# Optimization experiments

Measured on AMD Instinct MI355X. Metric: run time of the kernel, lower is better.

## Reference

```python
import jax, jax.numpy as jnp
import numpy as np

W_GLOBAL, W_SOFT, W_HARD = 0.2, 0.3, 0.5
GAMMA, ALPHA = 2.0, 0.25
MIN_TEMP, MAX_TEMP = 0.01, 100.0
EPS = 1e-12


def _l2norm(x, axis):
    n = jnp.sqrt(jnp.sum(x * x, axis=axis, keepdims=True))
    return x / jnp.maximum(n, EPS)


def _focal_ce(logits, labels):
    # torch F.cross_entropy with label_smoothing=ALPHA, then focal modulation
    log_p = jax.nn.log_softmax(logits, axis=-1)           # (B, K)
    nll = -jnp.take_along_axis(log_p, labels[:, None], axis=-1)[:, 0]
    smooth = -jnp.mean(log_p, axis=-1)
    ce = (1.0 - ALPHA) * nll + ALPHA * smooth
    pt = jnp.exp(-ce)
    return jnp.mean((1.0 - pt) ** GAMMA * ce)


def setup_inputs() -> dict:
    key = jax.random.key(0)
    k1, k2, k3 = jax.random.split(key, 3)
    B, C, N = 256, 512, 512
    yolo_feats = jax.random.normal(k1, (B, C, N), dtype=jnp.float32)
    clip_feats = jax.random.normal(k2, (B, C), dtype=jnp.float32)
    logit_scale = jax.random.uniform(k3, (1,), dtype=jnp.float32) * 2.0 + 2.0
    return {"yolo_feats": yolo_feats, "clip_feats": clip_feats, "logit_scale": logit_scale}


def reference(yolo_feats, clip_feats, logit_scale):
    yolo_feats = _l2norm(yolo_feats, axis=1)              # (B, C, N)
    clip_feats = _l2norm(clip_feats, axis=1)              # (B, C)
    scale = jnp.clip(jnp.exp(logit_scale), MIN_TEMP, MAX_TEMP)  # (1,)
    B = yolo_feats.shape[0]
    labels = jnp.arange(B, dtype=jnp.int32)

    # global branch
    yolo_global = _l2norm(jnp.mean(yolo_feats, axis=2), axis=1)   # (B, C)
    sim_global = (yolo_global @ clip_feats.T) * scale             # (B, B)
    loss_global = 0.5 * (_focal_ce(sim_global, labels) + _focal_ce(sim_global.T, labels))

    # dense spatial similarity map (B, N, K=B)
    sim_map = jnp.einsum('bcn,kc->bnk', yolo_feats, clip_feats) * scale

    sim_soft = jax.nn.logsumexp(sim_map, axis=1)                  # (B, B)
    loss_soft = 0.5 * (_focal_ce(sim_soft, labels) + _focal_ce(sim_soft.T, labels))

    sim_hard = jnp.max(sim_map, axis=1)                           # (B, B)
    loss_hard = 0.5 * (_focal_ce(sim_hard, labels) + _focal_ce(sim_hard.T, labels))

    return W_GLOBAL * loss_global + W_SOFT * loss_soft + W_HARD * loss_hard
```

## Files before the change

kernel.cpp:

```cpp
#include <hip/hip_runtime.h>
#include <math.h>

constexpr int B = 256;
constexpr int C = 512;
constexpr int N = 512;
constexpr int K = 256;

constexpr size_t OFF_CLIPNB = 0;
constexpr size_t OFF_INV    = OFF_CLIPNB + (size_t)B*C/2;
constexpr size_t OFF_SGLOB  = OFF_INV   + (size_t)B*N;
constexpr size_t OFF_SSOFT  = OFF_SGLOB + (size_t)B*K;
constexpr size_t OFF_SHARD  = OFF_SSOFT + (size_t)B*K;
constexpr size_t OFF_PM     = OFF_SHARD + (size_t)B*K;
constexpr size_t OFF_PS     = OFF_PM    + (size_t)2*B*K;
constexpr size_t OFF_PH     = OFF_PS    + (size_t)2*B*K;
constexpr size_t OFF_PG     = OFF_PH    + (size_t)2*B*K;
constexpr size_t OFF_GN     = OFF_PG    + (size_t)2*B*K;
constexpr size_t OFF_MISC   = OFF_GN    + (size_t)B;

typedef __attribute__((ext_vector_type(8))) short short8;
typedef __attribute__((ext_vector_type(4))) float f32x4;

__device__ __forceinline__ float wave_reduce_sum(float v) {
  #pragma unroll
  for (int off = 32; off > 0; off >>= 1) v += __shfl_xor(v, off, 64);
  return v;
}
__device__ __forceinline__ float wave_reduce_max(float v) {
  #pragma unroll
  for (int off = 32; off > 0; off >>= 1) v = fmaxf(v, __shfl_xor(v, off, 64));
  return v;
}
__device__ __forceinline__ unsigned int bf16_rne(float x) {
  unsigned int u = __builtin_bit_cast(unsigned int, x);
  return (u + 0x7FFFu + ((u >> 16) & 1u)) >> 16;
}
__device__ __forceinline__ unsigned int pk_bf16(float x, float y) {
  return bf16_rne(x) | (bf16_rne(y) << 16);
}

__global__ void k_misc(const float* __restrict__ ls, float* __restrict__ misc) {
  int t = threadIdx.x;
  if (t == 0) misc[0] = fminf(fmaxf(expf(ls[0]), 0.01f), 100.0f);
  if (t >= 1 && t < 7) misc[t] = 0.0f;
}

__global__ __launch_bounds__(256) void k_rownorm(const float* __restrict__ src,
                                                 unsigned short* __restrict__ dst_bf) {
  int b = blockIdx.x, t = threadIdx.x;
  float x0 = src[(size_t)b * C + t];
  float x1 = src[(size_t)b * C + t + 256];
  __shared__ float red[4];
  float w = wave_reduce_sum(x0 * x0 + x1 * x1);
  if ((t & 63) == 0) red[t >> 6] = w;
  __syncthreads();
  float tot = red[0] + red[1] + red[2] + red[3];
  float r = 1.0f / fmaxf(sqrtf(tot), 1e-12f);
  dst_bf[(size_t)b * C + t] = (unsigned short)bf16_rne(x0 * r);
  dst_bf[(size_t)b * C + t + 256] = (unsigned short)bf16_rne(x1 * r);
}

__global__ __launch_bounds__(256, 2) void k_main_mfma(
    const float* __restrict__ yolo,
    const unsigned short* __restrict__ clipnb,
    const float* __restrict__ misc,
    float* __restrict__ invg,
    float* __restrict__ PM, float* __restrict__ PS, float* __restrict__ PH,
    float* __restrict__ PG) {
  int bh = blockIdx.x;
  int b = bh >> 1, half = bh & 1;
  int t = threadIdx.x;
  int w = t >> 6, lane = t & 63;
  int quad = lane >> 4, col = lane & 15;

  __shared__ unsigned int xl[128 * 32];
  __shared__ float ssqb[8 * 128];
  __shared__ float invt[128];

  const float scale = misc[0];
  const float* ybase = yolo + (size_t)b * C * N;

  int nf = t & 31;
  int cp0 = t >> 5;
  unsigned int rotv = (8u * (nf & 3) + 4u * (unsigned)(nf >> 2)) & 31u;

  float msk[16], ssk[16], hsk[16];
  #pragma unroll
  for (int i = 0; i < 16; i++) { msk[i] = -1e30f; ssk[i] = 0.f; hsk[i] = -1e30f; }

  for (int iter = 0; iter < 2; iter++) {
    int n0 = half * 256 + iter * 128;
    float4 ssq4 = {0.f, 0.f, 0.f, 0.f};

    f32x4 acc[4][8];
    #pragma unroll
    for (int kt = 0; kt < 4; kt++)
      #pragma unroll
      for (int nt = 0; nt < 8; nt++) {
        f32x4 z = {0.f, 0.f, 0.f, 0.f};
        acc[kt][nt] = z;
      }

    for (int cc = 0; cc < 8; cc++) {
      int c0 = cc * 64;
      __syncthreads();

      short8 afr[4][2];
      #pragma unroll
      for (int kt = 0; kt < 4; kt++)
        #pragma unroll
        for (int s = 0; s < 2; s++) {
          const unsigned short* ap =
              clipnb + (size_t)(64 * w + 16 * kt + col) * C + c0 + 32 * s + 8 * quad;
          union { uint4 u; short8 v; } fa;
          fa.u = *(const uint4*)ap;
          afr[kt][s] = fa.v;
        }

      #pragma unroll
      for (int p = 0; p < 4; p++) {
        int cp = cp0 + 8 * p;
        int c = c0 + 2 * cp;
        const float* pa = ybase + (size_t)c * N + n0 + 4 * nf;
        float4 a = *(const float4*)pa;
        float4 bb = *(const float4*)(pa + N);
        ssq4.x += a.x * a.x + bb.x * bb.x;
        ssq4.y += a.y * a.y + bb.y * bb.y;
        ssq4.z += a.z * a.z + bb.z * bb.z;
        ssq4.w += a.w * a.w + bb.w * bb.w;
        unsigned int pos = ((unsigned)cp + rotv) & 31u;
        int base0 = (4 * nf) * 32;
        xl[base0 + pos]       = pk_bf16(a.x, bb.x);
        xl[base0 + 32 + pos]  = pk_bf16(a.y, bb.y);
        xl[base0 + 64 + pos]  = pk_bf16(a.z, bb.z);
        xl[base0 + 96 + pos]  = pk_bf16(a.w, bb.w);
      }
      __syncthreads();

      #pragma unroll
      for (int s = 0; s < 2; s++) {
        #pragma unroll
        for (int nt = 0; nt < 8; nt++) {
          int n = 16 * nt + col;
          unsigned int pos =
              (unsigned)(16 * s + 4 * quad + 8 * (col >> 2) + 4 * nt) & 31u;
          union { uint4 u; short8 v; } fb;
          fb.u = *(const uint4*)&xl[n * 32 + pos];
          #pragma unroll
          for (int kt = 0; kt < 4; kt++)
            acc[kt][nt] = __builtin_amdgcn_mfma_f32_16x16x32_bf16(
                afr[kt][s], fb.v, acc[kt][nt], 0, 0, 0);
        }
      }
    }

    {
      int base = cp0 * 128 + 4 * nf;
      ssqb[base + 0] = ssq4.x;
      ssqb[base + 1] = ssq4.y;
      ssqb[base + 2] = ssq4.z;
      ssqb[base + 3] = ssq4.w;
    }
    __syncthreads();
    if (t < 128) {
      float s = 0.f;
      #pragma unroll
      for (int g = 0; g < 8; g++) s += ssqb[g * 128 + t];
      float iv = 1.0f / fmaxf(sqrtf(s), 1e-12f);
      invt[t] = iv;
      invg[(size_t)b * N + n0 + t] = iv;
    }
    __syncthreads();

    float invn[8];
    #pragma unroll
    for (int nt = 0; nt < 8; nt++) invn[nt] = invt[16 * nt + col];
    #pragma unroll
    for (int kt = 0; kt < 4; kt++)
      #pragma unroll
      for (int r = 0; r < 4; r++) {
        int idx = kt * 4 + r;
        float mm = msk[idx], ss = ssk[idx], hh = hsk[idx], gg = 0.f;
        #pragma unroll
        for (int nt = 0; nt < 8; nt++) {
          float vu = acc[kt][nt][r] * invn[nt];
          gg += vu;
          float v = vu * scale;
          hh = fmaxf(hh, v);
          float M = fmaxf(mm, v);
          ss = ss * __expf(mm - M) + __expf(v - M);
          mm = M;
        }
        msk[idx] = mm; ssk[idx] = ss; hsk[idx] = hh;
        #pragma unroll
        for (int o = 1; o < 16; o <<= 1) gg += __shfl_xor(gg, o, 64);
        if (col == 0) {
          size_t a = (size_t)bh * 256 + (64 * w + 16 * kt + 4 * quad + r);
          if (iter == 0) PG[a] = gg; else PG[a] += gg;
        }
      }
  }

  #pragma unroll
  for (int idx = 0; idx < 16; idx++) {
    float mm = msk[idx], ss = ssk[idx], hh = hsk[idx];
    #pragma unroll
    for (int o = 1; o < 16; o <<= 1) {
      float mo = __shfl_xor(mm, o, 64);
      float so = __shfl_xor(ss, o, 64);
      float ho = __shfl_xor(hh, o, 64);
      float M = fmaxf(mm, mo);
      ss = ss * __expf(mm - M) + so * __expf(mo - M);
      mm = M;
      hh = fmaxf(hh, ho);
    }
    msk[idx] = mm; ssk[idx] = ss; hsk[idx] = hh;
  }
  if (col == 0) {
    size_t pbase = (size_t)bh * 256;
    #pragma unroll
    for (int kt = 0; kt < 4; kt++)
      #pragma unroll
      for (int r = 0; r < 4; r++) {
        int k = 64 * w + 16 * kt + 4 * quad + r;
        int idx = kt * 4 + r;
        PM[pbase + k] = msk[idx];
        PS[pbase + k] = ssk[idx];
        PH[pbase + k] = hsk[idx];
      }
  }
}

__global__ __launch_bounds__(512) void k_gnorm(const float* __restrict__ yolo,
                                               const float* __restrict__ invg,
                                               float* __restrict__ gn) {
  int b = blockIdx.x;
  int t = threadIdx.x;
  int w = t >> 6, lane = t & 63;
  const float* xb = yolo + (size_t)b * C * N;
  const float* ivb = invg + (size_t)b * N;
  float4 iv[2];
  #pragma unroll
  for (int p = 0; p < 2; p++) iv[p] = *(const float4*)(ivb + p * 256 + 4 * lane);
  float sq = 0.f;
  for (int ci = 0; ci < 64; ci++) {
    int c = w * 64 + ci;
    const float* row = xb + (size_t)c * N + 4 * lane;
    float cs = 0.f;
    #pragma unroll
    for (int p = 0; p < 2; p++) {
      float4 v = *(const float4*)(row + p * 256);
      cs += v.x * iv[p].x + v.y * iv[p].y + v.z * iv[p].z + v.w * iv[p].w;
    }
    cs = wave_reduce_sum(cs);
    sq += cs * cs;
  }
  __shared__ float red[8];
  if (lane == 0) red[w] = sq;
  __syncthreads();
  if (t == 0) {
    float s = 0.f;
    #pragma unroll
    for (int g = 0; g < 8; g++) s += red[g];
    gn[b] = fmaxf(sqrtf(s) * (1.0f / (float)N), 1e-12f);
  }
}

__global__ __launch_bounds__(256) void k_sglob(const float* __restrict__ PG,
                                               const float* __restrict__ gn,
                                               const float* __restrict__ misc,
                                               float* __restrict__ Sglob) {
  int i = blockIdx.x, k = threadIdx.x;
  float v = PG[(size_t)(2 * i) * 256 + k] + PG[(size_t)(2 * i + 1) * 256 + k];
  Sglob[(size_t)i * K + k] = misc[0] * v * (1.0f / (float)N) / gn[i];
}

__global__ __launch_bounds__(256) void k_merge(const float* __restrict__ PM,
                                               const float* __restrict__ PS,
                                               const float* __restrict__ PH,
                                               float* __restrict__ Ssoft,
                                               float* __restrict__ Shard) {
  int b = blockIdx.x, k = threadIdx.x;
  size_t p0 = (size_t)(2 * b) * 256 + k;
  size_t p1 = (size_t)(2 * b + 1) * 256 + k;
  float m0 = PM[p0], m1 = PM[p1];
  float M = fmaxf(m0, m1);
  float S = PS[p0] * __expf(m0 - M) + PS[p1] * __expf(m1 - M);
  Ssoft[(size_t)b * K + k] = M + __logf(S);
  Shard[(size_t)b * K + k] = fmaxf(PH[p0], PH[p1]);
}

__global__ __launch_bounds__(256) void k_focal(const float* __restrict__ Sglob,
                                               const float* __restrict__ Ssoft,
                                               const float* __restrict__ Shard,
                                               float* __restrict__ misc) {
  int job = blockIdx.y;
  int i = blockIdx.x;
  int t = threadIdx.x;
  const float* M = job < 2 ? Sglob : (job < 4 ? Ssoft : Shard);
  float v = (job & 1) ? M[(size_t)t * K + i] : M[(size_t)i * K + t];
  __shared__ float red[4];
  float mx = wave_reduce_max(v);
  if ((t & 63) == 0) red[t >> 6] = mx;
  __syncthreads();
  mx = fmaxf(fmaxf(red[0], red[1]), fmaxf(red[2], red[3]));
  __syncthreads();
  float sv = wave_reduce_sum(v);
  if ((t & 63) == 0) red[t >> 6] = sv;
  __syncthreads();
  float sumv = red[0] + red[1] + red[2] + red[3];
  __syncthreads();
  float se = wave_reduce_sum(expf(v - mx));
  if ((t & 63) == 0) red[t >> 6] = se;
  __syncthreads();
  if (t == 0) {
    float sumexp = red[0] + red[1] + red[2] + red[3];
    float logZ = mx + logf(sumexp);
    float diag = M[(size_t)i * K + i];
    float nll = logZ - diag;
    float smooth = logZ - sumv * (1.0f / 256.0f);
    float ce = 0.75f * nll + 0.25f * smooth;
    float pt = expf(-ce);
    float fo = (1.0f - pt) * (1.0f - pt) * ce;
    atomicAdd(&misc[1 + job], fo);
  }
}

__global__ void k_finish(const float* __restrict__ misc, float* __restrict__ out) {
  float lg = misc[1] + misc[2];
  float ls = misc[3] + misc[4];
  float lh = misc[5] + misc[6];
  out[0] = (0.2f * lg + 0.3f * ls + 0.5f * lh) * 0.5f * (1.0f / 256.0f);
}

extern "C" void kernel_launch(void* const* d_in, const int* in_sizes, int n_in,
                              void* d_out, int out_size, void* d_ws, size_t ws_size,
                              hipStream_t stream) {
  const float* yolo = (const float*)d_in[0];
  const float* clip = (const float*)d_in[1];
  const float* ls   = (const float*)d_in[2];
  float* out = (float*)d_out;
  float* ws = (float*)d_ws;
  unsigned short* clipnb = (unsigned short*)(ws + OFF_CLIPNB);
  float* invg  = ws + OFF_INV;
  float* Sglob = ws + OFF_SGLOB;
  float* Ssoft = ws + OFF_SSOFT;
  float* Shard = ws + OFF_SHARD;
  float* PM    = ws + OFF_PM;
  float* PS    = ws + OFF_PS;
  float* PH    = ws + OFF_PH;
  float* PG    = ws + OFF_PG;
  float* gn    = ws + OFF_GN;
  float* misc  = ws + OFF_MISC;

  k_misc<<<1, 64, 0, stream>>>(ls, misc);
  k_rownorm<<<256, 256, 0, stream>>>(clip, clipnb);
  k_main_mfma<<<512, 256, 0, stream>>>(yolo, clipnb, misc, invg, PM, PS, PH, PG);
  k_gnorm<<<256, 512, 0, stream>>>(yolo, invg, gn);
  k_sglob<<<256, 256, 0, stream>>>(PG, gn, misc, Sglob);
  k_merge<<<256, 256, 0, stream>>>(PM, PS, PH, Ssoft, Shard);
  k_focal<<<dim3(256, 6), 256, 0, stream>>>(Sglob, Ssoft, Shard, misc);
  k_finish<<<1, 1, 0, stream>>>(misc, out);
}
```

Before: 477.4 us.

## Stage full-C yolo windows in LDS, use 32x32 MFMA, fuse global-norm pass

The main kernel now splits each batch into four 128-column windows. Each block loads the whole C dimension of its window into LDS once as bf16 and computes the per-column inverse norms before the MFMA loop. The loop switches from 16x16x32 to 32x32x16 bf16 MFMA tiles, with no per-chunk syncs. The per-channel mean needed for the global branch is computed from the already staged LDS data, so the separate k_gnorm pass that re-read all of yolo from HBM is gone. The hard max is reused from the running max, so PH is no longer written. In exchange, merge kernels read 8 partials instead of 2, LDS use is much larger (128 KB), and the global mean now uses bf16-rounded values.

```diff
diff --git a/kernel.cpp b/kernel.cpp
--- a/kernel.cpp
+++ b/kernel.cpp
@@ -5,21 +5,21 @@
 constexpr int C = 512;
 constexpr int N = 512;
 constexpr int K = 256;
+constexpr int WIN = 128;
 
 constexpr size_t OFF_CLIPNB = 0;
-constexpr size_t OFF_INV    = OFF_CLIPNB + (size_t)B*C/2;
-constexpr size_t OFF_SGLOB  = OFF_INV   + (size_t)B*N;
+constexpr size_t OFF_SGLOB  = OFF_CLIPNB + (size_t)B*C/2;
 constexpr size_t OFF_SSOFT  = OFF_SGLOB + (size_t)B*K;
 constexpr size_t OFF_SHARD  = OFF_SSOFT + (size_t)B*K;
 constexpr size_t OFF_PM     = OFF_SHARD + (size_t)B*K;
-constexpr size_t OFF_PS     = OFF_PM    + (size_t)2*B*K;
-constexpr size_t OFF_PH     = OFF_PS    + (size_t)2*B*K;
-constexpr size_t OFF_PG     = OFF_PH    + (size_t)2*B*K;
-constexpr size_t OFF_GN     = OFF_PG    + (size_t)2*B*K;
+constexpr size_t OFF_PS     = OFF_PM    + (size_t)8*B*K;
+constexpr size_t OFF_PG     = OFF_PS    + (size_t)8*B*K;
+constexpr size_t OFF_S1     = OFF_PG    + (size_t)8*B*K;
+constexpr size_t OFF_GN     = OFF_S1    + (size_t)2048*512;
 constexpr size_t OFF_MISC   = OFF_GN    + (size_t)B;
 
-typedef __attribute__((ext_vector_type(8))) short short8;
-typedef __attribute__((ext_vector_type(4))) float f32x4;
+typedef __attribute__((ext_vector_type(8)))  short short8;
+typedef __attribute__((ext_vector_type(16))) float f32x16;
 
 __device__ __forceinline__ float wave_reduce_sum(float v) {
   #pragma unroll
@@ -60,208 +60,160 @@
   dst_bf[(size_t)b * C + t + 256] = (unsigned short)bf16_rne(x1 * r);
 }
 
-__global__ __launch_bounds__(256, 2) void k_main_mfma(
+__global__ __launch_bounds__(512, 2) void k_main2(
     const float* __restrict__ yolo,
     const unsigned short* __restrict__ clipnb,
     const float* __restrict__ misc,
-    float* __restrict__ invg,
-    float* __restrict__ PM, float* __restrict__ PS, float* __restrict__ PH,
-    float* __restrict__ PG) {
-  int bh = blockIdx.x;
-  int b = bh >> 1, half = bh & 1;
+    float* __restrict__ PM, float* __restrict__ PS, float* __restrict__ PG,
+    float* __restrict__ S1p) {
+  int bw = blockIdx.x;
+  int b = bw >> 2, win = bw & 3;
   int t = threadIdx.x;
   int w = t >> 6, lane = t & 63;
-  int quad = lane >> 4, col = lane & 15;
-
-  __shared__ unsigned int xl[128 * 32];
-  __shared__ float ssqb[8 * 128];
-  __shared__ float invt[128];
+  int half = lane >> 5, nl = lane & 31;
+  int kq = w & 3, ng = w >> 2;
+
+  __shared__ unsigned int xl[WIN * 256];
+  __shared__ float ssqb[16 * WIN];
+  __shared__ float invt[WIN];
 
   const float scale = misc[0];
-  const float* ybase = yolo + (size_t)b * C * N;
-
-  int nf = t & 31;
-  int cp0 = t >> 5;
-  unsigned int rotv = (8u * (nf & 3) + 4u * (unsigned)(nf >> 2)) & 31u;
-
-  float msk[16], ssk[16], hsk[16];
-  #pragma unroll
-  for (int i = 0; i < 16; i++) { msk[i] = -1e30f; ssk[i] = 0.f; hsk[i] = -1e30f; }
-
-  for (int iter = 0; iter < 2; iter++) {
-    int n0 = half * 256 + iter * 128;
+  const float* ybase = yolo + (size_t)b * C * N + win * WIN;
+
+  {
+    int nf = t & 31, cq = t >> 5;
+    int row = 4 * nf;
+    unsigned rw = 16u * (nf & 1) + 8u * ((nf >> 1) & 1);
     float4 ssq4 = {0.f, 0.f, 0.f, 0.f};
-
-    f32x4 acc[4][8];
+    #pragma unroll 4
+    for (int p = 0; p < 16; p++) {
+      int cp = cq + 16 * p;
+      const float* pa = ybase + (size_t)(2 * cp) * N + 4 * nf;
+      float4 a  = *(const float4*)pa;
+      float4 bb = *(const float4*)(pa + N);
+      ssq4.x += a.x * a.x + bb.x * bb.x;
+      ssq4.y += a.y * a.y + bb.y * bb.y;
+      ssq4.z += a.z * a.z + bb.z * bb.z;
+      ssq4.w += a.w * a.w + bb.w * bb.w;
+      int bhi = cp & ~31;
+      xl[(row + 0) * 256 + bhi + (int)(((unsigned)cp + rw +  0u) & 31u)] = pk_bf16(a.x, bb.x);
+      xl[(row + 1) * 256 + bhi + (int)(((unsigned)cp + rw +  4u) & 31u)] = pk_bf16(a.y, bb.y);
+      xl[(row + 2) * 256 + bhi + (int)(((unsigned)cp + rw +  8u) & 31u)] = pk_bf16(a.z, bb.z);
+      xl[(row + 3) * 256 + bhi + (int)(((unsigned)cp + rw + 12u) & 31u)] = pk_bf16(a.w, bb.w);
+    }
+    ssqb[cq * WIN + row + 0] = ssq4.x;
+    ssqb[cq * WIN + row + 1] = ssq4.y;
+    ssqb[cq * WIN + row + 2] = ssq4.z;
+    ssqb[cq * WIN + row + 3] = ssq4.w;
+  }
+  __syncthreads();
+  if (t < WIN) {
+    float s = 0.f;
     #pragma unroll
-    for (int kt = 0; kt < 4; kt++)
+    for (int g = 0; g < 16; g++) s += ssqb[g * WIN + t];
+    invt[t] = 1.0f / fmaxf(sqrtf(s), 1e-12f);
+  }
+  __syncthreads();
+
+  int kt0 = kq, kt1 = kq + 4;
+  int nt0 = 2 * ng, nt1 = 2 * ng + 1;
+  const unsigned short* a0p = clipnb + (size_t)(32 * kt0 + nl) * C + 8 * half;
+  const unsigned short* a1p = clipnb + (size_t)(32 * kt1 + nl) * C + 8 * half;
+  int brow0 = (32 * nt0 + nl) * 256;
+  int brow1 = (32 * nt1 + nl) * 256;
+  unsigned rotr = 4u * ((unsigned)(nl & 3) + 4u * ((nl >> 2) & 1) + 2u * ((nl >> 3) & 1));
+
+  f32x16 acc00, acc01, acc10, acc11;
+  #pragma unroll
+  for (int r = 0; r < 16; r++) { acc00[r] = 0.f; acc01[r] = 0.f; acc10[r] = 0.f; acc11[r] = 0.f; }
+
+  #pragma unroll 4
+  for (int step = 0; step < 32; step++) {
+    union { uint4 u; short8 v; } A0, A1, B0, B1;
+    A0.u = *(const uint4*)(a0p + 16 * step);
+    A1.u = *(const uint4*)(a1p + 16 * step);
+    int pos = 32 * (step >> 2) +
+              (int)(((unsigned)(8 * (step & 3) + 4 * half) + rotr) & 31u);
+    B0.u = *(const uint4*)&xl[brow0 + pos];
+    B1.u = *(const uint4*)&xl[brow1 + pos];
+    acc00 = __builtin_amdgcn_mfma_f32_32x32x16_bf16(A0.v, B0.v, acc00, 0, 0, 0);
+    acc01 = __builtin_amdgcn_mfma_f32_32x32x16_bf16(A0.v, B1.v, acc01, 0, 0, 0);
+    acc10 = __builtin_amdgcn_mfma_f32_32x32x16_bf16(A1.v, B0.v, acc10, 0, 0, 0);
+    acc11 = __builtin_amdgcn_mfma_f32_32x32x16_bf16(A1.v, B1.v, acc11, 0, 0, 0);
+  }
+
+  float ivr0 = invt[32 * nt0 + nl];
+  float ivr1 = invt[32 * nt1 + nl];
+  size_t pb = ((size_t)b * 8 + win * 2 + ng) * 256;
+  #pragma unroll
+  for (int tk = 0; tk < 2; tk++) {
+    int kbase = 32 * (tk ? kt1 : kt0);
+    #pragma unroll
+    for (int reg = 0; reg < 16; reg++) {
+      float u0 = (tk ? acc10[reg] : acc00[reg]) * ivr0;
+      float u1 = (tk ? acc11[reg] : acc01[reg]) * ivr1;
+      float v0 = u0 * scale, v1 = u1 * scale;
+      float M = fmaxf(v0, v1);
+      float G = u0 + u1;
       #pragma unroll
-      for (int nt = 0; nt < 8; nt++) {
-        f32x4 z = {0.f, 0.f, 0.f, 0.f};
-        acc[kt][nt] = z;
+      for (int o = 1; o < 32; o <<= 1) M = fmaxf(M, __shfl_xor(M, o, 64));
+      float e = __expf(v0 - M) + __expf(v1 - M);
+      #pragma unroll
+      for (int o = 1; o < 32; o <<= 1) {
+        e += __shfl_xor(e, o, 64);
+        G += __shfl_xor(G, o, 64);
       }
-
-    for (int cc = 0; cc < 8; cc++) {
-      int c0 = cc * 64;
-      __syncthreads();
-
-      short8 afr[4][2];
-      #pragma unroll
-      for (int kt = 0; kt < 4; kt++)
-        #pragma unroll
-        for (int s = 0; s < 2; s++) {
-          const unsigned short* ap =
-              clipnb + (size_t)(64 * w + 16 * kt + col) * C + c0 + 32 * s + 8 * quad;
-          union { uint4 u; short8 v; } fa;
-          fa.u = *(const uint4*)ap;
-          afr[kt][s] = fa.v;
-        }
-
-      #pragma unroll
-      for (int p = 0; p < 4; p++) {
-        int cp = cp0 + 8 * p;
-        int c = c0 + 2 * cp;
-        const float* pa = ybase + (size_t)c * N + n0 + 4 * nf;
-        float4 a = *(const float4*)pa;
-        float4 bb = *(const float4*)(pa + N);
-        ssq4.x += a.x * a.x + bb.x * bb.x;
-        ssq4.y += a.y * a.y + bb.y * bb.y;
-        ssq4.z += a.z * a.z + bb.z * bb.z;
-        ssq4.w += a.w * a.w + bb.w * bb.w;
-        unsigned int pos = ((unsigned)cp + rotv) & 31u;
-        int base0 = (4 * nf) * 32;
-        xl[base0 + pos]       = pk_bf16(a.x, bb.x);
-        xl[base0 + 32 + pos]  = pk_bf16(a.y, bb.y);
-        xl[base0 + 64 + pos]  = pk_bf16(a.z, bb.z);
-        xl[base0 + 96 + pos]  = pk_bf16(a.w, bb.w);
-      }
-      __syncthreads();
-
-      #pragma unroll
-      for (int s = 0; s < 2; s++) {
-        #pragma unroll
-        for (int nt = 0; nt < 8; nt++) {
-          int n = 16 * nt + col;
-          unsigned int pos =
-              (unsigned)(16 * s + 4 * quad + 8 * (col >> 2) + 4 * nt) & 31u;
-          union { uint4 u; short8 v; } fb;
-          fb.u = *(const uint4*)&xl[n * 32 + pos];
-          #pragma unroll
-          for (int kt = 0; kt < 4; kt++)
-            acc[kt][nt] = __builtin_amdgcn_mfma_f32_16x16x32_bf16(
-                afr[kt][s], fb.v, acc[kt][nt], 0, 0, 0);
-        }
+      if (nl == 0) {
+        int k = kbase + (reg & 3) + 8 * (reg >> 2) + 4 * half;
+        PM[pb + k] = M;
+        PS[pb + k] = e;
+        PG[pb + k] = G;
       }
     }
-
-    {
-      int base = cp0 * 128 + 4 * nf;
-      ssqb[base + 0] = ssq4.x;
-      ssqb[base + 1] = ssq4.y;
-      ssqb[base + 2] = ssq4.z;
-      ssqb[base + 3] = ssq4.w;
+  }
+
+  {
+    int cp2 = t >> 1, sub = t & 1;
+    int qhi = cp2 & ~31, qlo = cp2 & 31;
+    float s0 = 0.f, s1 = 0.f;
+    #pragma unroll 16
+    for (int i = 0; i < 64; i++) {
+      int n = 64 * sub + i;
+      unsigned rt = 4u * (unsigned)(i & 3) + 16u * ((i >> 2) & 1) + 8u * ((i >> 3) & 1);
+      unsigned dw = xl[n * 256 + qhi + (int)(((unsigned)qlo + rt) & 31u)];
+      float iv = invt[n];
+      float xlo = __builtin_bit_cast(float, dw << 16);
+      float xhi = __builtin_bit_cast(float, dw & 0xffff0000u);
+      s0 = fmaf(xlo, iv, s0);
+      s1 = fmaf(xhi, iv, s1);
     }
-    __syncthreads();
-    if (t < 128) {
-      float s = 0.f;
-      #pragma unroll
-      for (int g = 0; g < 8; g++) s += ssqb[g * 128 + t];
-      float iv = 1.0f / fmaxf(sqrtf(s), 1e-12f);
-      invt[t] = iv;
-      invg[(size_t)b * N + n0 + t] = iv;
-    }
-    __syncthreads();
-
-    float invn[8];
-    #pragma unroll
-    for (int nt = 0; nt < 8; nt++) invn[nt] = invt[16 * nt + col];
-    #pragma unroll
-    for (int kt = 0; kt < 4; kt++)
-      #pragma unroll
-      for (int r = 0; r < 4; r++) {
-        int idx = kt * 4 + r;
-        float mm = msk[idx], ss = ssk[idx], hh = hsk[idx], gg = 0.f;
-        #pragma unroll
-        for (int nt = 0; nt < 8; nt++) {
-          float vu = acc[kt][nt][r] * invn[nt];
-          gg += vu;
-          float v = vu * scale;
-          hh = fmaxf(hh, v);
-          float M = fmaxf(mm, v);
-          ss = ss * __expf(mm - M) + __expf(v - M);
-          mm = M;
-        }
-        msk[idx] = mm; ssk[idx] = ss; hsk[idx] = hh;
-        #pragma unroll
-        for (int o = 1; o < 16; o <<= 1) gg += __shfl_xor(gg, o, 64);
-        if (col == 0) {
-          size_t a = (size_t)bh * 256 + (64 * w + 16 * kt + 4 * quad + r);
-          if (iter == 0) PG[a] = gg; else PG[a] += gg;
-        }
-      }
-  }
-
-  #pragma unroll
-  for (int idx = 0; idx < 16; idx++) {
-    float mm = msk[idx], ss = ssk[idx], hh = hsk[idx];
-    #pragma unroll
-    for (int o = 1; o < 16; o <<= 1) {
-      float mo = __shfl_xor(mm, o, 64);
-      float so = __shfl_xor(ss, o, 64);
-      float ho = __shfl_xor(hh, o, 64);
-      float M = fmaxf(mm, mo);
-      ss = ss * __expf(mm - M) + so * __expf(mo - M);
-      mm = M;
-      hh = fmaxf(hh, ho);
-    }
-    msk[idx] = mm; ssk[idx] = ss; hsk[idx] = hh;
-  }
-  if (col == 0) {
-    size_t pbase = (size_t)bh * 256;
-    #pragma unroll
-    for (int kt = 0; kt < 4; kt++)
-      #pragma unroll
-      for (int r = 0; r < 4; r++) {
-        int k = 64 * w + 16 * kt + 4 * quad + r;
-        int idx = kt * 4 + r;
-        PM[pbase + k] = msk[idx];
-        PS[pbase + k] = ssk[idx];
-        PH[pbase + k] = hsk[idx];
-      }
-  }
-}
-
-__global__ __launch_bounds__(512) void k_gnorm(const float* __restrict__ yolo,
-                                               const float* __restrict__ invg,
-                                               float* __restrict__ gn) {
-  int b = blockIdx.x;
-  int t = threadIdx.x;
-  int w = t >> 6, lane = t & 63;
-  const float* xb = yolo + (size_t)b * C * N;
-  const float* ivb = invg + (size_t)b * N;
-  float4 iv[2];
-  #pragma unroll
-  for (int p = 0; p < 2; p++) iv[p] = *(const float4*)(ivb + p * 256 + 4 * lane);
-  float sq = 0.f;
-  for (int ci = 0; ci < 64; ci++) {
-    int c = w * 64 + ci;
-    const float* row = xb + (size_t)c * N + 4 * lane;
-    float cs = 0.f;
-    #pragma unroll
-    for (int p = 0; p < 2; p++) {
-      float4 v = *(const float4*)(row + p * 256);
-      cs += v.x * iv[p].x + v.y * iv[p].y + v.z * iv[p].z + v.w * iv[p].w;
-    }
-    cs = wave_reduce_sum(cs);
-    sq += cs * cs;
-  }
-  __shared__ float red[8];
-  if (lane == 0) red[w] = sq;
-  __syncthreads();
-  if (t == 0) {
+    size_t o = ((size_t)bw * 2 + sub) * 512 + 2 * cp2;
+    S1p[o] = s0;
+    S1p[o + 1] = s1;
+  }
+}
+
+__global__ __launch_bounds__(256) void k_gn2(const float* __restrict__ S1p,
+                                             float* __restrict__ gn) {
+  int b = blockIdx.x, t = threadIdx.x;
+  float tot = 0.f;
+  #pragma unroll
+  for (int cc = 0; cc < 2; cc++) {
+    int c = t + 256 * cc;
     float s = 0.f;
     #pragma unroll
-    for (int g = 0; g < 8; g++) s += red[g];
+    for (int wn = 0; wn < 4; wn++)
+      #pragma unroll
+      for (int sub = 0; sub < 2; sub++)
+        s += S1p[(((size_t)(b * 4 + wn)) * 2 + sub) * 512 + c];
+    tot += s * s;
+  }
+  __shared__ float red[4];
+  float wsum = wave_reduce_sum(tot);
+  if ((t & 63) == 0) red[t >> 6] = wsum;
+  __syncthreads();
+  if (t == 0) {
+    float s = red[0] + red[1] + red[2] + red[3];
     gn[b] = fmaxf(sqrtf(s) * (1.0f / (float)N), 1e-12f);
   }
 }
@@ -271,23 +223,28 @@
                                                const float* __restrict__ misc,
                                                float* __restrict__ Sglob) {
   int i = blockIdx.x, k = threadIdx.x;
-  float v = PG[(size_t)(2 * i) * 256 + k] + PG[(size_t)(2 * i + 1) * 256 + k];
+  float v = 0.f;
+  #pragma unroll
+  for (int p = 0; p < 8; p++) v += PG[((size_t)i * 8 + p) * 256 + k];
   Sglob[(size_t)i * K + k] = misc[0] * v * (1.0f / (float)N) / gn[i];
 }
 
 __global__ __launch_bounds__(256) void k_merge(const float* __restrict__ PM,
                                                const float* __restrict__ PS,
-                                               const float* __restrict__ PH,
                                                float* __restrict__ Ssoft,
                                                float* __restrict__ Shard) {
   int b = blockIdx.x, k = threadIdx.x;
-  size_t p0 = (size_t)(2 * b) * 256 + k;
-  size_t p1 = (size_t)(2 * b + 1) * 256 + k;
-  float m0 = PM[p0], m1 = PM[p1];
-  float M = fmaxf(m0, m1);
-  float S = PS[p0] * __expf(m0 - M) + PS[p1] * __expf(m1 - M);
+  float M = -1e30f;
+  #pragma unroll
+  for (int p = 0; p < 8; p++) M = fmaxf(M, PM[((size_t)b * 8 + p) * 256 + k]);
+  float S = 0.f;
+  #pragma unroll
+  for (int p = 0; p < 8; p++) {
+    size_t o = ((size_t)b * 8 + p) * 256 + k;
+    S += PS[o] * __expf(PM[o] - M);
+  }
   Ssoft[(size_t)b * K + k] = M + __logf(S);
-  Shard[(size_t)b * K + k] = fmaxf(PH[p0], PH[p1]);
+  Shard[(size_t)b * K + k] = M;
 }
 
 __global__ __launch_bounds__(256) void k_focal(const float* __restrict__ Sglob,
@@ -342,23 +299,22 @@
   float* out = (float*)d_out;
   float* ws = (float*)d_ws;
   unsigned short* clipnb = (unsigned short*)(ws + OFF_CLIPNB);
-  float* invg  = ws + OFF_INV;
   float* Sglob = ws + OFF_SGLOB;
   float* Ssoft = ws + OFF_SSOFT;
   float* Shard = ws + OFF_SHARD;
   float* PM    = ws + OFF_PM;
   float* PS    = ws + OFF_PS;
-  float* PH    = ws + OFF_PH;
   float* PG    = ws + OFF_PG;
+  float* S1p   = ws + OFF_S1;
   float* gn    = ws + OFF_GN;
   float* misc  = ws + OFF_MISC;
 
   k_misc<<<1, 64, 0, stream>>>(ls, misc);
   k_rownorm<<<256, 256, 0, stream>>>(clip, clipnb);
-  k_main_mfma<<<512, 256, 0, stream>>>(yolo, clipnb, misc, invg, PM, PS, PH, PG);
-  k_gnorm<<<256, 512, 0, stream>>>(yolo, invg, gn);
+  k_main2<<<1024, 512, 0, stream>>>(yolo, clipnb, misc, PM, PS, PG, S1p);
+  k_gn2<<<256, 256, 0, stream>>>(S1p, gn);
   k_sglob<<<256, 256, 0, stream>>>(PG, gn, misc, Sglob);
-  k_merge<<<256, 256, 0, stream>>>(PM, PS, PH, Ssoft, Shard);
+  k_merge<<<256, 256, 0, stream>>>(PM, PS, Ssoft, Shard);
   k_focal<<<dim3(256, 6), 256, 0, stream>>>(Sglob, Ssoft, Shard, misc);
   k_finish<<<1, 1, 0, stream>>>(misc, out);
 }
```

New measurement: 500.9 us. 4.9% more time.
